# Kernel optimization log

Hardware: AMD Instinct MI355X
Metric: run time of the kernel (lower is better)

Reference implementation:

```python
import jax, jax.numpy as jnp
import numpy as np

A = 9  # len(scales) * len(ratios) anchor templates
DN = ('NHWC', 'HWIO', 'NHWC')


def _conv(x, w, b):
    y = jax.lax.conv_general_dilated(x, w, window_strides=(1, 1), padding='SAME',
                                     dimension_numbers=DN)
    return y + b


def setup_inputs() -> dict:
    key = jax.random.key(0)
    ks = jax.random.split(key, 9)
    s = 0.02  # weight init scale
    x = jax.random.normal(ks[0], (4, 128, 128, 512), jnp.float32)
    W1 = jax.random.normal(ks[1], (3, 3, 512, 256), jnp.float32) * s
    b1 = jnp.zeros((256,), jnp.float32)
    W2 = jax.random.normal(ks[2], (3, 3, 256, 256), jnp.float32) * s
    b2 = jnp.zeros((256,), jnp.float32)
    Wr = jax.random.normal(ks[3], (1, 1, 256, 4 * A), jnp.float32) * s
    br = jnp.zeros((4 * A,), jnp.float32)
    Wc = jax.random.normal(ks[4], (1, 1, 256, 2 * A), jnp.float32) * s
    bc = jnp.zeros((2 * A,), jnp.float32)
    return {'x': x, 'W1': W1, 'b1': b1, 'W2': W2, 'b2': b2,
            'Wr': Wr, 'br': br, 'Wc': Wc, 'bc': bc}


def reference(x, W1, b1, W2, b2, Wr, br, Wc, bc):
    h = jax.nn.relu(_conv(x, W1, b1))
    h = jax.nn.relu(_conv(h, W2, b2))
    B, H, W = h.shape[0], h.shape[1], h.shape[2]
    reg = _conv(h, Wr, br).reshape(B, H, W, A, 4)            # (B,H,W,A,4)
    cls = _conv(h, Wc, bc).reshape(B, H, W, A, 2)            # (B,H,W,A,2)
    cls = jax.nn.softmax(cls, axis=4)
    return jnp.concatenate((cls, reg), axis=4)               # (B,H,W,A,6)
```

## Files before the change

### kernel.cpp

```cpp
#include <hip/hip_runtime.h>


typedef float f32x4  __attribute__((ext_vector_type(4)));
typedef float f32x16 __attribute__((ext_vector_type(16)));
typedef short bf16x8 __attribute__((ext_vector_type(8)));

union U16x8 { uint4 v; unsigned short s[8]; };

__device__ __forceinline__ unsigned short f2bf(float f) {
  union { float f; unsigned int u; } v; v.f = f;
  unsigned int r = v.u + 0x7FFFu + ((v.u >> 16) & 1u);
  return (unsigned short)(r >> 16);
}

__global__ __launch_bounds__(256) void transpose_cvt(
    const float* __restrict__ src, unsigned short* __restrict__ dst,
    int K, int N) {
  __shared__ float t[32][33];
  const int tx = threadIdx.x, ty = threadIdx.y;
  const int k0 = blockIdx.x * 32, n0 = blockIdx.y * 32;
  const float* s = src + (size_t)blockIdx.z * K * N;
  unsigned short* d = dst + (size_t)blockIdx.z * N * K;
#pragma unroll
  for (int r = 0; r < 32; r += 8) {
    int k = k0 + ty + r, n = n0 + tx;
    t[ty + r][tx] = (k < K && n < N) ? s[(size_t)k * N + n] : 0.f;
  }
  __syncthreads();
#pragma unroll
  for (int r = 0; r < 32; r += 8) {
    int n = n0 + ty + r, k = k0 + tx;
    if (n < N && k < K) d[(size_t)n * K + k] = f2bf(t[tx][ty + r]);
  }
}

__global__ __launch_bounds__(256) void convert_x(
    const float* __restrict__ x, unsigned short* __restrict__ xp) {
  int idx = blockIdx.x * 256 + threadIdx.x;
  int g = idx & 63;
  int cell = idx >> 6;
  int xpix = cell % 130;
  int t = cell / 130;
  int ypix = t % 130;
  int b = t / 130;
  U16x8 u;
  if (xpix == 0 || xpix == 129 || ypix == 0 || ypix == 129) {
    u.v = make_uint4(0u, 0u, 0u, 0u);
  } else {
    const float* sp = x + ((size_t)((b * 128 + ypix - 1) * 128) + (xpix - 1)) * 512 + g * 8;
    float4 a = *(const float4*)sp;
    float4 c = *(const float4*)(sp + 4);
    u.s[0] = f2bf(a.x); u.s[1] = f2bf(a.y); u.s[2] = f2bf(a.z); u.s[3] = f2bf(a.w);
    u.s[4] = f2bf(c.x); u.s[5] = f2bf(c.y); u.s[6] = f2bf(c.z); u.s[7] = f2bf(c.w);
  }
  *(uint4*)(xp + (size_t)cell * 512 + g * 8) = u.v;
}

__global__ __launch_bounds__(256) void zero_h1_borders(unsigned short* __restrict__ h1p) {
  int idx = blockIdx.x * 256 + threadIdx.x;
  int g = idx & 31;
  int cell = idx >> 5;
  int xpix = cell % 130;
  int t = cell / 130;
  int ypix = t % 130;
  if (xpix == 0 || xpix == 129 || ypix == 0 || ypix == 129)
    *(uint4*)(h1p + (size_t)cell * 256 + g * 8) = make_uint4(0u, 0u, 0u, 0u);
}

template<int CIN, int MODE>
__global__ __launch_bounds__(256) void conv3x3(
    const unsigned short* __restrict__ Ap,
    const unsigned short* __restrict__ WT,
    const float* __restrict__ bias,
    unsigned short* __restrict__ out) {
  __shared__ __align__(16) unsigned short As[130][72];
  __shared__ __align__(16) unsigned short Bs[3][128][72];
  const int tid  = threadIdx.x;
  const int wave = tid >> 6, lane = tid & 63;
  const int wm = wave >> 1, wn = wave & 1;
  const int l31 = lane & 31, hi = lane >> 5;
  const int b = blockIdx.x >> 7, y = blockIdx.x & 127;
  const int nbase = blockIdx.y * 128;

  f32x16 acc[2][2] = {};

  for (int dy = 0; dy < 3; ++dy) {
    const unsigned short* Arow = Ap + ((size_t)(b * 130 + y + dy) * 130) * CIN;
    const unsigned short* Btap = WT + ((size_t)(dy * 3) * 256 + nbase) * CIN;
    for (int ci0 = 0; ci0 < CIN; ci0 += 64) {
      for (int s = tid; s < 1040; s += 256) {
        int row = s >> 3, seg = s & 7;
        *(uint4*)&As[row][seg * 8] =
            *(const uint4*)(Arow + (size_t)row * CIN + ci0 + seg * 8);
      }
#pragma unroll
      for (int t = 0; t < 12; ++t) {
        int s = t * 256 + tid;
        int dx = s >> 10, r = (s >> 3) & 127, seg = s & 7;
        *(uint4*)&Bs[dx][r][seg * 8] =
            *(const uint4*)(Btap + ((size_t)dx * 256 + r) * CIN + ci0 + seg * 8);
      }
      __syncthreads();
#pragma unroll
      for (int dx = 0; dx < 3; ++dx) {
#pragma unroll
        for (int ks = 0; ks < 4; ++ks) {
          bf16x8 af[2], bfr[2];
#pragma unroll
          for (int i = 0; i < 2; ++i)
            af[i] = *(const bf16x8*)&As[wm * 64 + i * 32 + l31 + dx][ks * 16 + hi * 8];
#pragma unroll
          for (int j = 0; j < 2; ++j)
            bfr[j] = *(const bf16x8*)&Bs[dx][wn * 64 + j * 32 + l31][ks * 16 + hi * 8];
#pragma unroll
          for (int i = 0; i < 2; ++i)
#pragma unroll
            for (int j = 0; j < 2; ++j)
              acc[i][j] = __builtin_amdgcn_mfma_f32_32x32x16_bf16(af[i], bfr[j], acc[i][j], 0, 0, 0);
        }
      }
      __syncthreads();
    }
  }

#pragma unroll
  for (int i = 0; i < 2; ++i) {
#pragma unroll
    for (int j = 0; j < 2; ++j) {
      int n = nbase + wn * 64 + j * 32 + l31;
      float bb = bias[n];
#pragma unroll
      for (int reg = 0; reg < 16; ++reg) {
        int m = wm * 64 + i * 32 + (reg & 3) + 8 * (reg >> 2) + 4 * hi;
        float v = fmaxf(acc[i][j][reg] + bb, 0.f);
        size_t off;
        if (MODE == 0)
          off = ((size_t)(b * 130 + y + 1) * 130 + (m + 1)) * 256 + n;
        else
          off = ((size_t)((b * 128 + y) * 128 + m)) * 256 + n;
        out[off] = f2bf(v);
      }
    }
  }
}

__global__ __launch_bounds__(256) void heads_kernel(
    const unsigned short* __restrict__ h2,
    const unsigned short* __restrict__ WhT,
    const float* __restrict__ br, const float* __restrict__ bc,
    float* __restrict__ out) {
  __shared__ __align__(16) unsigned short As[64][264];
  const int tid = threadIdx.x;
  const int wave = tid >> 6, lane = tid & 63;
  const int quad = lane >> 4, l16 = lane & 15;
  const int pix0 = blockIdx.x * 64;
#pragma unroll
  for (int r = 0; r < 8; ++r) {
    int s = r * 256 + tid;
    int row = s >> 5, seg = s & 31;
    *(uint4*)&As[row][seg * 8] =
        *(const uint4*)(h2 + (size_t)(pix0 + row) * 256 + seg * 8);
  }
  __syncthreads();
  f32x4 acc[4] = {};
#pragma unroll
  for (int ks = 0; ks < 8; ++ks) {
    bf16x8 af = *(const bf16x8*)&As[wave * 16 + l16][ks * 32 + quad * 8];
#pragma unroll
    for (int j = 0; j < 4; ++j) {
      bf16x8 bfr = *(const bf16x8*)(WhT + (size_t)(j * 16 + l16) * 256 + ks * 32 + quad * 8);
      acc[j] = __builtin_amdgcn_mfma_f32_16x16x32_bf16(af, bfr, acc[j], 0, 0, 0);
    }
  }
#pragma unroll
  for (int j = 0; j < 4; ++j) {
    int n = j * 16 + l16;
    float bias = 0.f;
    if (n < 18) bias = bc[n];
    else if (n < 54) bias = br[n - 18];
#pragma unroll
    for (int r = 0; r < 4; ++r) {
      int p = pix0 + wave * 16 + quad * 4 + r;
      float v = acc[j][r] + bias;
      float partner = __shfl_xor(v, 1);
      if (n < 18) {
        float mx = fmaxf(v, partner);
        float e0 = __expf(v - mx), e1 = __expf(partner - mx);
        int a = n >> 1, sl = n & 1;
        out[(size_t)p * 54 + a * 6 + sl] = e0 / (e0 + e1);
      } else if (n < 54) {
        int rr = n - 18, a = rr >> 2, sl = (rr & 3) + 2;
        out[(size_t)p * 54 + a * 6 + sl] = v;
      }
    }
  }
}

extern "C" void kernel_launch(void* const* d_in, const int* in_sizes, int n_in,
                              void* d_out, int out_size, void* d_ws, size_t ws_size,
                              hipStream_t stream) {
  const float* x  = (const float*)d_in[0];
  const float* W1 = (const float*)d_in[1];
  const float* b1 = (const float*)d_in[2];
  const float* W2 = (const float*)d_in[3];
  const float* b2 = (const float*)d_in[4];
  const float* Wr = (const float*)d_in[5];
  const float* br = (const float*)d_in[6];
  const float* Wc = (const float*)d_in[7];
  const float* bc = (const float*)d_in[8];
  float* out = (float*)d_out;

  constexpr size_t XPAD_B  = 4ull * 130 * 130 * 512 * 2;
  constexpr size_t H1PAD_B = 4ull * 130 * 130 * 256 * 2;
  constexpr size_t H2_B    = 4ull * 128 * 128 * 256 * 2;
  constexpr size_t W1T_B   = 9ull * 256 * 512 * 2;
  constexpr size_t W2T_B   = 9ull * 256 * 256 * 2;
  char* ws = (char*)d_ws;
  unsigned short* x_pad  = (unsigned short*)(ws);
  unsigned short* h1_pad = (unsigned short*)(ws + XPAD_B);
  unsigned short* h2     = (unsigned short*)(ws + XPAD_B + H1PAD_B);
  unsigned short* W1T    = (unsigned short*)(ws + XPAD_B + H1PAD_B + H2_B);
  unsigned short* W2T    = (unsigned short*)(ws + XPAD_B + H1PAD_B + H2_B + W1T_B);
  unsigned short* WhT    = (unsigned short*)(ws + XPAD_B + H1PAD_B + H2_B + W1T_B + W2T_B);

  hipMemsetAsync(WhT, 0, 64ull * 256 * 2, stream);
  transpose_cvt<<<dim3(16, 8, 9), dim3(32, 8), 0, stream>>>(W1, W1T, 512, 256);
  transpose_cvt<<<dim3(8, 8, 9),  dim3(32, 8), 0, stream>>>(W2, W2T, 256, 256);
  transpose_cvt<<<dim3(8, 1, 1),  dim3(32, 8), 0, stream>>>(Wc, WhT, 256, 18);
  transpose_cvt<<<dim3(8, 2, 1),  dim3(32, 8), 0, stream>>>(Wr, WhT + 18 * 256, 256, 36);
  convert_x<<<16900, 256, 0, stream>>>(x, x_pad);
  zero_h1_borders<<<8450, 256, 0, stream>>>(h1_pad);
  conv3x3<512, 0><<<dim3(512, 2), 256, 0, stream>>>(x_pad, W1T, b1, h1_pad);
  conv3x3<256, 1><<<dim3(512, 2), 256, 0, stream>>>(h1_pad, W2T, b2, h2);
  heads_kernel<<<1024, 256, 0, stream>>>(h2, WhT, br, bc, out);
}
```

Measured before the change: 510.7 us.

## Restructure conv3x3 with async global-to-LDS double buffering and larger tiles

Rewrites the 3x3 conv kernel so that 512-thread blocks each compute two output rows across all 256 output channels. Operands are staged with global_load_lds directly into XOR-swizzled, double-buffered shared memory, so the next K-slice loads while the current one computes. The explicit vmcnt waits and barriers replace the old load-then-sync pattern. This aims to hide global latency, cut LDS bank conflicts and reuse weights across two rows, at the cost of fewer blocks (256) and higher register and LDS pressure.

```diff
diff --git a/kernel.cpp b/kernel.cpp
--- a/kernel.cpp
+++ b/kernel.cpp
@@ -12,6 +12,11 @@
   unsigned int r = v.u + 0x7FFFu + ((v.u >> 16) & 1u);
   return (unsigned short)(r >> 16);
 }
+
+#define GLOAD_LDS16(G, L)                                        \
+  __builtin_amdgcn_global_load_lds(                              \
+      (const __attribute__((address_space(1))) void*)(G),        \
+      (__attribute__((address_space(3))) void*)(L), 16, 0, 0)
 
 __global__ __launch_bounds__(256) void transpose_cvt(
     const float* __restrict__ src, unsigned short* __restrict__ dst,
@@ -68,76 +73,126 @@
 }
 
 template<int CIN, int MODE>
-__global__ __launch_bounds__(256) void conv3x3(
+__global__ __launch_bounds__(512, 2) void conv3x3(
     const unsigned short* __restrict__ Ap,
     const unsigned short* __restrict__ WT,
     const float* __restrict__ bias,
     unsigned short* __restrict__ out) {
-  __shared__ __align__(16) unsigned short As[130][72];
-  __shared__ __align__(16) unsigned short Bs[3][128][72];
+  constexpr int NCI    = CIN / 32;
+  constexpr int LOGNCI = (NCI == 16) ? 4 : 3;
+  constexpr int NT     = 3 * NCI;
+  constexpr int A_BYTES = 2 * 192 * 4 * 16;
+  constexpr int B_BYTES = 3 * 256 * 4 * 16;
+  constexpr int BUF     = A_BYTES + B_BYTES;
+  __shared__ __align__(16) unsigned char smem[2 * BUF];
+
   const int tid  = threadIdx.x;
   const int wave = tid >> 6, lane = tid & 63;
-  const int wm = wave >> 1, wn = wave & 1;
   const int l31 = lane & 31, hi = lane >> 5;
-  const int b = blockIdx.x >> 7, y = blockIdx.x & 127;
-  const int nbase = blockIdx.y * 128;
-
-  f32x16 acc[2][2] = {};
-
-  for (int dy = 0; dy < 3; ++dy) {
-    const unsigned short* Arow = Ap + ((size_t)(b * 130 + y + dy) * 130) * CIN;
-    const unsigned short* Btap = WT + ((size_t)(dy * 3) * 256 + nbase) * CIN;
-    for (int ci0 = 0; ci0 < CIN; ci0 += 64) {
-      for (int s = tid; s < 1040; s += 256) {
-        int row = s >> 3, seg = s & 7;
-        *(uint4*)&As[row][seg * 8] =
-            *(const uint4*)(Arow + (size_t)row * CIN + ci0 + seg * 8);
+  const int wm = wave >> 2, wn = wave & 3;
+  const int b = blockIdx.x >> 6;
+  const int y0 = (blockIdx.x & 63) * 2;
+  const int brow = b * 130 + y0;
+
+  int a_go[3], a_ld[3];
+#pragma unroll
+  for (int i = 0; i < 3; ++i) {
+    int s = (wave * 3 + i) * 64 + lane;
+    int br = (s >= 768) ? 1 : 0;
+    int r = s - br * 768;
+    int px = r >> 2, sl = r & 3;
+    a_go[i] = (br * 130 + px) * CIN + ((sl ^ ((px >> 1) & 3)) * 8);
+    a_ld[i] = (wave * 3 + i) * 1024;
+  }
+  int b_go[6], b_ld[6];
+#pragma unroll
+  for (int i = 0; i < 6; ++i) {
+    int s = (wave * 6 + i) * 64 + lane;
+    int dxs = s >> 10, r = s & 1023;
+    int co = r >> 2, sl = r & 3;
+    b_go[i] = (dxs * 256 + co) * CIN + ((sl ^ ((co >> 1) & 3)) * 8);
+    b_ld[i] = A_BYTES + (wave * 6 + i) * 1024;
+  }
+
+  const float bb0 = bias[wn * 64 + l31];
+  const float bb1 = bias[wn * 64 + 32 + l31];
+
+  f32x16 acc[4][2] = {};
+  const int bswz = (l31 >> 1) & 3;
+
+  auto stage = [&](int tile) {
+    const int dy  = tile >> LOGNCI;
+    const int ci0 = (tile & (NCI - 1)) << 5;
+    unsigned char* sb = smem + (size_t)(tile & 1) * BUF;
+    const unsigned short* Ab = Ap + (size_t)(brow + dy) * 130 * CIN + ci0;
+#pragma unroll
+    for (int i = 0; i < 3; ++i)
+      GLOAD_LDS16(Ab + a_go[i], sb + a_ld[i]);
+    const unsigned short* Bb = WT + (size_t)dy * 3 * 256 * CIN + ci0;
+#pragma unroll
+    for (int i = 0; i < 6; ++i)
+      GLOAD_LDS16(Bb + b_go[i], sb + b_ld[i]);
+  };
+
+  auto compute = [&](int t) {
+    const unsigned char* sb = smem + (size_t)(t & 1) * BUF;
+#pragma unroll
+    for (int dx = 0; dx < 3; ++dx) {
+      const int aswz  = ((l31 + dx) >> 1) & 3;
+      const int abase = wm * 12288 + (l31 + dx) * 64;
+      const int bbase = A_BYTES + dx * 16384 + wn * 4096 + l31 * 64;
+#pragma unroll
+      for (int ks = 0; ks < 2; ++ks) {
+        const int q = ks * 2 + hi;
+        bf16x8 af[4], bfr[2];
+        const int ab = abase + ((q ^ aswz) * 16);
+#pragma unroll
+        for (int i = 0; i < 4; ++i)
+          af[i] = *(const bf16x8*)(sb + ab + i * 2048);
+        const int bby = bbase + ((q ^ bswz) * 16);
+#pragma unroll
+        for (int j = 0; j < 2; ++j)
+          bfr[j] = *(const bf16x8*)(sb + bby + j * 2048);
+#pragma unroll
+        for (int i = 0; i < 4; ++i)
+#pragma unroll
+          for (int j = 0; j < 2; ++j)
+            acc[i][j] = __builtin_amdgcn_mfma_f32_32x32x16_bf16(af[i], bfr[j], acc[i][j], 0, 0, 0);
       }
-#pragma unroll
-      for (int t = 0; t < 12; ++t) {
-        int s = t * 256 + tid;
-        int dx = s >> 10, r = (s >> 3) & 127, seg = s & 7;
-        *(uint4*)&Bs[dx][r][seg * 8] =
-            *(const uint4*)(Btap + ((size_t)dx * 256 + r) * CIN + ci0 + seg * 8);
-      }
-      __syncthreads();
-#pragma unroll
-      for (int dx = 0; dx < 3; ++dx) {
-#pragma unroll
-        for (int ks = 0; ks < 4; ++ks) {
-          bf16x8 af[2], bfr[2];
-#pragma unroll
-          for (int i = 0; i < 2; ++i)
-            af[i] = *(const bf16x8*)&As[wm * 64 + i * 32 + l31 + dx][ks * 16 + hi * 8];
-#pragma unroll
-          for (int j = 0; j < 2; ++j)
-            bfr[j] = *(const bf16x8*)&Bs[dx][wn * 64 + j * 32 + l31][ks * 16 + hi * 8];
-#pragma unroll
-          for (int i = 0; i < 2; ++i)
-#pragma unroll
-            for (int j = 0; j < 2; ++j)
-              acc[i][j] = __builtin_amdgcn_mfma_f32_32x32x16_bf16(af[i], bfr[j], acc[i][j], 0, 0, 0);
-        }
-      }
-      __syncthreads();
-    }
-  }
-
-#pragma unroll
-  for (int i = 0; i < 2; ++i) {
+    }
+  };
+
+  stage(0);
+#pragma unroll 2
+  for (int t = 0; t < NT - 1; ++t) {
+    stage(t + 1);
+    asm volatile("s_waitcnt vmcnt(9)" ::: "memory");
+    __builtin_amdgcn_s_barrier();
+    __builtin_amdgcn_sched_barrier(0);
+    compute(t);
+    __builtin_amdgcn_sched_barrier(0);
+    __builtin_amdgcn_s_barrier();
+  }
+  asm volatile("s_waitcnt vmcnt(0)" ::: "memory");
+  __builtin_amdgcn_s_barrier();
+  __builtin_amdgcn_sched_barrier(0);
+  compute(NT - 1);
+
+#pragma unroll
+  for (int i = 0; i < 4; ++i) {
 #pragma unroll
     for (int j = 0; j < 2; ++j) {
-      int n = nbase + wn * 64 + j * 32 + l31;
-      float bb = bias[n];
+      const int n = wn * 64 + j * 32 + l31;
+      const float bb = j ? bb1 : bb0;
 #pragma unroll
       for (int reg = 0; reg < 16; ++reg) {
-        int m = wm * 64 + i * 32 + (reg & 3) + 8 * (reg >> 2) + 4 * hi;
+        int px = i * 32 + (reg & 3) + 8 * (reg >> 2) + 4 * hi;
         float v = fmaxf(acc[i][j][reg] + bb, 0.f);
         size_t off;
         if (MODE == 0)
-          off = ((size_t)(b * 130 + y + 1) * 130 + (m + 1)) * 256 + n;
+          off = ((size_t)(brow + wm + 1) * 130 + (px + 1)) * 256 + n;
         else
-          off = ((size_t)((b * 128 + y) * 128 + m)) * 256 + n;
+          off = ((size_t)(b * 128 + y0 + wm) * 128 + px) * 256 + n;
         out[off] = f2bf(v);
       }
     }
@@ -230,7 +285,7 @@
   transpose_cvt<<<dim3(8, 2, 1),  dim3(32, 8), 0, stream>>>(Wr, WhT + 18 * 256, 256, 36);
   convert_x<<<16900, 256, 0, stream>>>(x, x_pad);
   zero_h1_borders<<<8450, 256, 0, stream>>>(h1_pad);
-  conv3x3<512, 0><<<dim3(512, 2), 256, 0, stream>>>(x_pad, W1T, b1, h1_pad);
-  conv3x3<256, 1><<<dim3(512, 2), 256, 0, stream>>>(h1_pad, W2T, b2, h2);
+  conv3x3<512, 0><<<256, 512, 0, stream>>>(x_pad, W1T, b1, h1_pad);
+  conv3x3<256, 1><<<256, 512, 0, stream>>>(h1_pad, W2T, b2, h2);
   heads_kernel<<<1024, 256, 0, stream>>>(h2, WhT, br, bc, out);
 }
```

After: 517.9 us. About the same (+1.4%).
